# Performance work log

Measured on AMD Instinct MI355X. Metric: run time of the kernel, lower is better.

The kernel has to match this reference:

```python
import jax, jax.numpy as jnp
import numpy as np

EMB = 768
HEADS = 8
HEAD_DIM = EMB // HEADS  # 96
B, N = 4, 2048


def setup_inputs() -> dict:
    key = jax.random.key(0)
    ks = jax.random.split(key, 9)
    s = 1.0 / np.sqrt(EMB)
    x = jax.random.normal(ks[0], (B, N, EMB), dtype=jnp.float32)
    Wq = jax.random.uniform(ks[1], (EMB, EMB), jnp.float32, -s, s)
    bq = jax.random.uniform(ks[2], (EMB,), jnp.float32, -s, s)
    Wk = jax.random.uniform(ks[3], (EMB, EMB), jnp.float32, -s, s)
    bk = jax.random.uniform(ks[4], (EMB,), jnp.float32, -s, s)
    Wv = jax.random.uniform(ks[5], (EMB, EMB), jnp.float32, -s, s)
    bv = jax.random.uniform(ks[6], (EMB,), jnp.float32, -s, s)
    Wo = jax.random.uniform(ks[7], (EMB, EMB), jnp.float32, -s, s)
    bo = jax.random.uniform(ks[8], (EMB,), jnp.float32, -s, s)
    return {"x": x, "Wq": Wq, "bq": bq, "Wk": Wk, "bk": bk,
            "Wv": Wv, "bv": bv, "Wo": Wo, "bo": bo}


def _split_heads(t):
    b, n, _ = t.shape
    return t.reshape(b, n, HEADS, HEAD_DIM).transpose(0, 2, 1, 3)  # b h n d


def reference(x, Wq, bq, Wk, bk, Wv, bv, Wo, bo):
    q = _split_heads(x @ Wq + bq)
    k = _split_heads(x @ Wk + bk)
    v = _split_heads(x @ Wv + bv)
    # NOTE: faithful to source — softmax on UNSCALED logits, then divide by sqrt(head_dim)
    energy = jnp.einsum('bhqd,bhkd->bhqk', q, k)
    att = jax.nn.softmax(energy, axis=-1) / np.sqrt(HEAD_DIM)
    out = jnp.einsum('bhqk,bhkd->bhqd', att, v)
    out = out.transpose(0, 2, 1, 3).reshape(x.shape[0], x.shape[1], EMB)
    return out @ Wo + bo
```

## Files before the change

### kernel.cpp

```cpp
#include <hip/hip_runtime.h>

typedef _Float16 half_t;
typedef __attribute__((ext_vector_type(8))) _Float16 half8;
typedef __attribute__((ext_vector_type(2))) __fp16 fp16x2;
typedef __attribute__((ext_vector_type(4))) float f32x4;
typedef __attribute__((ext_vector_type(16))) float f32x16;

#define EMB 768
#define HEADS 8
#define HD 96
#define BB 4
#define NN 2048
#define BN (BB*NN)

static __device__ __forceinline__ f32x4 mfma16(half8 a, half8 b, f32x4 c) {
    return __builtin_amdgcn_mfma_f32_16x16x32_f16(a, b, c, 0, 0, 0);
}
static __device__ __forceinline__ f32x16 mfma32(half8 a, half8 b, f32x16 c) {
    return __builtin_amdgcn_mfma_f32_32x32x16_f16(a, b, c, 0, 0, 0);
}
static __device__ __forceinline__ unsigned pkrtz(float a, float b) {
    fp16x2 h = __builtin_amdgcn_cvt_pkrtz(a, b);
    return __builtin_bit_cast(unsigned, h);
}
static __device__ __forceinline__ unsigned sx32(unsigned v) {
    return (unsigned)__shfl_xor((int)v, 32);
}
static __device__ __forceinline__ float max3f(float a, float b, float c) {
    return fmaxf(fmaxf(a, b), c);
}
static __device__ __forceinline__ half8 pack8(float4 a, float4 b) {
    union { unsigned u[4]; half8 h; } t;
    t.u[0] = pkrtz(a.x, a.y); t.u[1] = pkrtz(a.z, a.w);
    t.u[2] = pkrtz(b.x, b.y); t.u[3] = pkrtz(b.z, b.w);
    return t.h;
}

__global__ __launch_bounds__(256) void cvt_transpose_w(
    const float* __restrict__ W0, const float* __restrict__ W1,
    const float* __restrict__ W2, const float* __restrict__ W3,
    half_t* __restrict__ T0, half_t* __restrict__ T1,
    half_t* __restrict__ T2, half_t* __restrict__ T3)
{
    const float* W; half_t* T;
    switch (blockIdx.z) {
        case 0: W = W0; T = T0; break;
        case 1: W = W1; T = T1; break;
        case 2: W = W2; T = T2; break;
        default: W = W3; T = T3; break;
    }
    __shared__ float ls[32][33];
    const int k0 = blockIdx.x * 32, n0 = blockIdx.y * 32;
    const int r = threadIdx.x >> 3, c4 = (threadIdx.x & 7) * 4;
    float4 v = *(const float4*)&W[(size_t)(k0 + r) * EMB + n0 + c4];
    ls[r][c4+0] = v.x; ls[r][c4+1] = v.y; ls[r][c4+2] = v.z; ls[r][c4+3] = v.w;
    __syncthreads();
    union { half_t h[4]; uint2 u; } t;
    #pragma unroll
    for (int j = 0; j < 4; ++j) t.h[j] = (half_t)ls[c4 + j][r];
    *(uint2*)&T[(size_t)(n0 + r) * EMB + k0 + c4] = t.u;
}

__global__ __launch_bounds__(256) void proj_qkv_h(
    const float* __restrict__ x,
    const half_t* __restrict__ WqT, const float* __restrict__ bq,
    const half_t* __restrict__ WkT, const float* __restrict__ bk,
    const half_t* __restrict__ WvT, const float* __restrict__ bv,
    half_t* __restrict__ Qo, half_t* __restrict__ Ko, half_t* __restrict__ Vt)
{
    const half_t* WT; const float* bias;
    const int z = blockIdx.z;
    if (z == 0)      { WT = WqT; bias = bq; }
    else if (z == 1) { WT = WkT; bias = bk; }
    else             { WT = WvT; bias = bv; }

    __shared__ half_t As[128][56];
    __shared__ half_t Bs[128][56];

    const int tid = threadIdx.x;
    const int lane = tid & 63;
    const int wid = tid >> 6;
    const int lr = lane & 15;
    const int lkg = lane >> 4;
    const int wm = (wid >> 1) * 64;
    const int wn = (wid & 1) * 64;
    const int mbase = blockIdx.x * 128;
    const int nbase = blockIdx.y * 128;

    const int srr = tid >> 2;
    const int skk = (tid & 3) * 8;

    f32x4 acc[4][4];
    const f32x4 z4 = {0.f, 0.f, 0.f, 0.f};
    #pragma unroll
    for (int i = 0; i < 4; ++i)
        #pragma unroll
        for (int j = 0; j < 4; ++j) acc[i][j] = z4;

    const float*  aptr = x  + (size_t)(mbase + srr) * EMB + skk;
    const half_t* bptr = WT + (size_t)(nbase + srr) * EMB + skk;

    half8 a0 = pack8(*(const float4*)(aptr),
                     *(const float4*)(aptr + 4));
    half8 a1 = pack8(*(const float4*)(aptr + 64 * EMB),
                     *(const float4*)(aptr + 64 * EMB + 4));
    half8 b0 = *(const half8*)bptr;
    half8 b1 = *(const half8*)(bptr + 64 * EMB);

    for (int k0 = 0; k0 < EMB; k0 += 32) {
        __syncthreads();
        *(half8*)&As[srr][skk]      = a0;
        *(half8*)&As[srr + 64][skk] = a1;
        *(half8*)&Bs[srr][skk]      = b0;
        *(half8*)&Bs[srr + 64][skk] = b1;
        __syncthreads();
        if (k0 + 32 < EMB) {
            a0 = pack8(*(const float4*)(aptr + k0 + 32),
                       *(const float4*)(aptr + k0 + 36));
            a1 = pack8(*(const float4*)(aptr + k0 + 32 + 64 * EMB),
                       *(const float4*)(aptr + k0 + 36 + 64 * EMB));
            b0 = *(const half8*)(bptr + k0 + 32);
            b1 = *(const half8*)(bptr + k0 + 32 + 64 * EMB);
        }
        half8 af[4], bf[4];
        #pragma unroll
        for (int mi = 0; mi < 4; ++mi)
            af[mi] = *(const half8*)&As[wm + mi*16 + lr][lkg*8];
        #pragma unroll
        for (int ni = 0; ni < 4; ++ni)
            bf[ni] = *(const half8*)&Bs[wn + ni*16 + lr][lkg*8];
        #pragma unroll
        for (int mi = 0; mi < 4; ++mi)
            #pragma unroll
            for (int ni = 0; ni < 4; ++ni)
                acc[mi][ni] = mfma16(af[mi], bf[ni], acc[mi][ni]);
    }

    const float qscale = (z == 0) ? 1.4426950408889634f : 1.0f;

    #pragma unroll
    for (int ni = 0; ni < 4; ++ni) {
        const int e = nbase + wn + ni*16 + lr;
        const float be = bias[e];
        const int h = e / HD, d = e % HD;
        #pragma unroll
        for (int mi = 0; mi < 4; ++mi) {
            const int row0 = mbase + wm + mi*16 + lkg*4;
            const int b = row0 >> 11, n0 = row0 & (NN - 1);
            if (z == 2) {
                union { half_t hh[4]; uint2 u; } t;
                #pragma unroll
                for (int r = 0; r < 4; ++r) t.hh[r] = (half_t)(acc[mi][ni][r] + be);
                *(uint2*)&Vt[((size_t)(b*HEADS + h) * HD + d) * NN + n0] = t.u;
            } else {
                half_t* outp = (z == 0) ? Qo : Ko;
                #pragma unroll
                for (int r = 0; r < 4; ++r)
                    outp[((size_t)(b*HEADS + h) * NN + n0 + r) * HD + d] =
                        (half_t)((acc[mi][ni][r] + be) * qscale);
            }
        }
    }
}

__global__ __launch_bounds__(256, 3) void attn_h(
    const half_t* __restrict__ Qh, const half_t* __restrict__ Kh,
    const half_t* __restrict__ Vth, half_t* __restrict__ AOh)
{
    __shared__ __align__(16) char smem[40960];

    const int tid = threadIdx.x;
    const int lane = tid & 63;
    const int wid = tid >> 6;
    const int l31 = lane & 31;
    const int b5 = lane >> 5;
    const int qsub = wid & 1;
    const int sub = wid >> 1;

    const int f = blockIdx.x;
    const int bh = (f & 7) + 8 * (f >> 8);
    const int qbase = ((f >> 3) & 31) * 64;

    const half_t* Qp = Qh + (size_t)bh * NN * HD;
    const half_t* Kp = Kh + (size_t)bh * NN * HD;
    const half_t* Vp = Vth + (size_t)bh * HD * NN;
    half_t* AOp = AOh + (size_t)bh * NN * HD;

    const int kr = tid >> 2;
    const int kcb = (tid & 3) * 48;
    const int vd = tid >> 1;
    const int vcb = (tid & 1) * 64;

    half8 kva, kvb, kvc, vv0, vv1, vv2, vv3;

#define KGLOAD(KT) {                                                          \
        const half_t* ksrc_ = Kp + (size_t)((KT) * 64 + kr) * HD + kcb / 2;   \
        kva = *(const half8*)(ksrc_);                                         \
        kvb = *(const half8*)(ksrc_ + 8);                                     \
        kvc = *(const half8*)(ksrc_ + 16); }
#define VGLOAD(KT) if (tid < 192) {                                           \
        const half_t* vsrc_ = Vp + (size_t)vd * NN + (KT) * 64 + vcb / 2;     \
        vv0 = *(const half8*)(vsrc_);      vv1 = *(const half8*)(vsrc_ + 8);  \
        vv2 = *(const half8*)(vsrc_ + 16); vv3 = *(const half8*)(vsrc_ + 24); }
#define WRITEBUF() {                                                          \
        char* kb_ = smem;                                                     \
        *(half8*)(kb_ + ((kr * 256 + kcb +  0) ^ ((kr & 15) << 4))) = kva;    \
        *(half8*)(kb_ + ((kr * 256 + kcb + 16) ^ ((kr & 15) << 4))) = kvb;    \
        *(half8*)(kb_ + ((kr * 256 + kcb + 32) ^ ((kr & 15) << 4))) = kvc;    \
        if (tid < 192) {                                                      \
            char* vb_ = smem + 16384;                                         \
            *(half8*)(vb_ + ((vd * 256 + vcb +  0) ^ ((vd & 15) << 4))) = vv0;\
            *(half8*)(vb_ + ((vd * 256 + vcb + 16) ^ ((vd & 15) << 4))) = vv1;\
            *(half8*)(vb_ + ((vd * 256 + vcb + 32) ^ ((vd & 15) << 4))) = vv2;\
            *(half8*)(vb_ + ((vd * 256 + vcb + 48) ^ ((vd & 15) << 4))) = vv3;\
        } }

    KGLOAD(0);
    VGLOAD(0);

    {
        const int r = tid >> 2;
        const int cb = (tid & 3) * 48;
        const half_t* src = Qp + (size_t)(qbase + r) * HD + cb / 2;
        #pragma unroll
        for (int c = 0; c < 3; ++c) {
            half8 q = *(const half8*)(src + c * 8);
            *(half8*)(smem + ((r * 256 + cb + c * 16) ^ ((r & 15) << 4))) = q;
        }
    }
    __syncthreads();
    half8 qf[6];
    {
        const int r = qsub * 32 + l31;
        #pragma unroll
        for (int kg = 0; kg < 6; ++kg)
            qf[kg] = *(const half8*)(smem + ((r * 256 + kg * 32 + 16 * b5) ^ ((r & 15) << 4)));
    }
    __syncthreads();

    f32x16 acc[3];
    const f32x16 z16 = {0.f,0.f,0.f,0.f,0.f,0.f,0.f,0.f,0.f,0.f,0.f,0.f,0.f,0.f,0.f,0.f};
    acc[0] = z16; acc[1] = z16; acc[2] = z16;
    float mreg = -1e30f, lreg = 0.f;

    const int kvrow = sub * 32 + l31;

    for (int kt = 0; kt < NN / 64; ++kt) {
        WRITEBUF();
        __syncthreads();

        if (kt + 1 < NN / 64) {
            KGLOAD(kt + 1);
            VGLOAD(kt + 1);
        }

        f32x16 st = z16;
        __builtin_amdgcn_s_setprio(1);
        #pragma unroll
        for (int kg = 0; kg < 6; ++kg) {
            half8 kf = *(const half8*)(smem +
                ((kvrow * 256 + kg * 32 + 16 * b5) ^ ((kvrow & 15) << 4)));
            st = mfma32(kf, qf[kg], st);
        }
        __builtin_amdgcn_s_setprio(0);

        const float t0 = max3f(st[0],  st[1],  st[2]);
        const float t1 = max3f(st[3],  st[4],  st[5]);
        const float t2 = max3f(st[6],  st[7],  st[8]);
        const float t3 = max3f(st[9],  st[10], st[11]);
        const float t4 = max3f(st[12], st[13], st[14]);
        const float tml = fmaxf(max3f(t0, t1, t2), max3f(t3, t4, st[15]));
        const float tm = fmaxf(tml, __shfl_xor(tml, 32));

        if (!__all(tm <= mreg + 8.0f)) {
            const float mn = fmaxf(mreg, tm);
            const float sc = exp2f(mreg - mn);
            lreg *= sc;
            #pragma unroll
            for (int db = 0; db < 3; ++db)
                #pragma unroll
                for (int i = 0; i < 16; ++i) acc[db][i] *= sc;
            mreg = mn;
        }

        float rs = 0.f;
        #pragma unroll
        for (int i = 0; i < 16; ++i) {
            const float p = exp2f(st[i] - mreg);
            st[i] = p;
            rs += p;
        }
        rs += __shfl_xor(rs, 32);
        lreg += rs;

        unsigned pk[4][2];
        #pragma unroll
        for (int rr = 0; rr < 4; ++rr) {
            pk[rr][0] = pkrtz(st[rr*4+0], st[rr*4+1]);
            pk[rr][1] = pkrtz(st[rr*4+2], st[rr*4+3]);
        }

        #pragma unroll
        for (int ks = 0; ks < 2; ++ks) {
            const unsigned z0 = b5 ? pk[2*ks][0] : pk[2*ks+1][0];
            const unsigned z1 = b5 ? pk[2*ks][1] : pk[2*ks+1][1];
            const unsigned x0 = sx32(z0);
            const unsigned x1 = sx32(z1);
            union { unsigned u[4]; half8 h; } afu;
            afu.u[0] = b5 ? x0 : pk[2*ks][0];
            afu.u[1] = b5 ? x1 : pk[2*ks][1];
            afu.u[2] = b5 ? pk[2*ks+1][0] : x0;
            afu.u[3] = b5 ? pk[2*ks+1][1] : x1;
            const half8 af = afu.h;
            __builtin_amdgcn_s_setprio(1);
            #pragma unroll
            for (int db = 0; db < 3; ++db) {
                const int d = db * 32 + l31;
                half8 vf = *(const half8*)(smem + 16384 +
                    ((d * 256 + sub * 64 + ks * 32 + 16 * b5) ^ ((d & 15) << 4)));
                acc[db] = mfma32(vf, af, acc[db]);
            }
            __builtin_amdgcn_s_setprio(0);
        }
        __syncthreads();
    }

#undef KGLOAD
#undef VGLOAD
#undef WRITEBUF

    float* fb = (float*)smem;
    fb[tid] = mreg;
    fb[256 + tid] = lreg;
    __syncthreads();
    const float mp = fb[tid ^ 128];
    const float lp = fb[256 + (tid ^ 128)];
    const float mc = fmaxf(mreg, mp);
    const float sc = exp2f(mreg - mc);
    const float lc = lreg * sc + lp * exp2f(mp - mc);
    __syncthreads();
    if (wid >= 2) {
        float* rec = fb + (qsub * 64 + lane) * 49;
        #pragma unroll
        for (int db = 0; db < 3; ++db)
            #pragma unroll
            for (int i = 0; i < 16; ++i) rec[db*16 + i] = acc[db][i] * sc;
    }
    __syncthreads();
    if (wid < 2) {
        const float* rec = fb + (qsub * 64 + lane) * 49;
        const float isq = 0.10206207261596577f;
        const float inv = isq / lc;
        const int q = qbase + qsub * 32 + l31;
        half_t* dst = AOp + (size_t)q * HD;
        #pragma unroll
        for (int db = 0; db < 3; ++db)
            #pragma unroll
            for (int rr = 0; rr < 4; ++rr) {
                const int d0 = db * 32 + rr * 8 + 4 * b5;
                union { half_t h[4]; uint2 u; } t;
                #pragma unroll
                for (int r = 0; r < 4; ++r)
                    t.h[r] = (half_t)((acc[db][rr*4 + r] * sc + rec[db*16 + rr*4 + r]) * inv);
                *(uint2*)&dst[d0] = t.u;
            }
    }
}

__global__ __launch_bounds__(256) void proj_out_h(
    const half_t* __restrict__ AOh, const half_t* __restrict__ WoT,
    const float* __restrict__ bo, float* __restrict__ out)
{
    __shared__ half_t As[128][56];
    __shared__ half_t Bs[128][56];

    const int tid = threadIdx.x;
    const int lane = tid & 63;
    const int wid = tid >> 6;
    const int lr = lane & 15;
    const int lkg = lane >> 4;
    const int wm = (wid >> 1) * 64;
    const int wn = (wid & 1) * 64;
    const int mbase = blockIdx.x * 128;
    const int nbase = blockIdx.y * 128;

    const int srr = tid >> 2;
    const int skk = (tid & 3) * 8;

    const int arow0 = mbase + srr;
    const int ab0 = arow0 >> 11, an0 = arow0 & (NN - 1);
    const int arow1 = arow0 + 64;
    const int ab1 = arow1 >> 11, an1 = arow1 & (NN - 1);

    f32x4 acc[4][4];
    const f32x4 z4 = {0.f, 0.f, 0.f, 0.f};
    #pragma unroll
    for (int i = 0; i < 4; ++i)
        #pragma unroll
        for (int j = 0; j < 4; ++j) acc[i][j] = z4;

    const half_t* bptr = WoT + (size_t)(nbase + srr) * EMB + skk;

#define ALOAD(b_, n_, k0_) \
    (*(const half8*)&AOh[((size_t)((b_)*HEADS + (k0_)/HD) * NN + (n_)) * HD + ((k0_)%HD) + skk])

    half8 a0 = ALOAD(ab0, an0, 0);
    half8 a1 = ALOAD(ab1, an1, 0);
    half8 b0 = *(const half8*)bptr;
    half8 b1 = *(const half8*)(bptr + 64 * EMB);

    for (int k0 = 0; k0 < EMB; k0 += 32) {
        __syncthreads();
        *(half8*)&As[srr][skk]      = a0;
        *(half8*)&As[srr + 64][skk] = a1;
        *(half8*)&Bs[srr][skk]      = b0;
        *(half8*)&Bs[srr + 64][skk] = b1;
        __syncthreads();
        if (k0 + 32 < EMB) {
            const int kn = k0 + 32;
            a0 = ALOAD(ab0, an0, kn);
            a1 = ALOAD(ab1, an1, kn);
            b0 = *(const half8*)(bptr + kn);
            b1 = *(const half8*)(bptr + kn + 64 * EMB);
        }
        half8 af[4], bf[4];
        #pragma unroll
        for (int mi = 0; mi < 4; ++mi)
            af[mi] = *(const half8*)&As[wm + mi*16 + lr][lkg*8];
        #pragma unroll
        for (int ni = 0; ni < 4; ++ni)
            bf[ni] = *(const half8*)&Bs[wn + ni*16 + lr][lkg*8];
        #pragma unroll
        for (int mi = 0; mi < 4; ++mi)
            #pragma unroll
            for (int ni = 0; ni < 4; ++ni)
                acc[mi][ni] = mfma16(af[mi], bf[ni], acc[mi][ni]);
    }
#undef ALOAD

    #pragma unroll
    for (int ni = 0; ni < 4; ++ni) {
        const int e = nbase + wn + ni*16 + lr;
        const float be = bo[e];
        #pragma unroll
        for (int mi = 0; mi < 4; ++mi) {
            const int row0 = mbase + wm + mi*16 + lkg*4;
            #pragma unroll
            for (int r = 0; r < 4; ++r)
                out[(size_t)(row0 + r) * EMB + e] = acc[mi][ni][r] + be;
        }
    }
}

extern "C" void kernel_launch(void* const* d_in, const int* in_sizes, int n_in,
                              void* d_out, int out_size, void* d_ws, size_t ws_size,
                              hipStream_t stream)
{
    const float* x  = (const float*)d_in[0];
    const float* Wq = (const float*)d_in[1];
    const float* bq = (const float*)d_in[2];
    const float* Wk = (const float*)d_in[3];
    const float* bk = (const float*)d_in[4];
    const float* Wv = (const float*)d_in[5];
    const float* bv = (const float*)d_in[6];
    const float* Wo = (const float*)d_in[7];
    const float* bo = (const float*)d_in[8];

    const size_t SZ = (size_t)BN * EMB;
    const size_t WS = (size_t)EMB * EMB;

    half_t* ws  = (half_t*)d_ws;
    half_t* WqT = ws;
    half_t* WkT = WqT + WS;
    half_t* WvT = WkT + WS;
    half_t* WoT = WvT + WS;
    half_t* Qh  = WoT + WS;
    half_t* Kh  = Qh  + SZ;
    half_t* Vth = Kh  + SZ;
    half_t* AOh = Vth + SZ;

    cvt_transpose_w<<<dim3(EMB/32, EMB/32, 4), 256, 0, stream>>>(
        Wq, Wk, Wv, Wo, WqT, WkT, WvT, WoT);

    proj_qkv_h<<<dim3(BN/128, EMB/128, 3), 256, 0, stream>>>(
        x, WqT, bq, WkT, bk, WvT, bv, Qh, Kh, Vth);

    attn_h<<<dim3((NN/64) * (BB*HEADS)), 256, 0, stream>>>(Qh, Kh, Vth, AOh);

    proj_out_h<<<dim3(BN/128, EMB/128), 256, 0, stream>>>(AOh, WoT, bo, (float*)d_out);
}
```

Baseline: 167.8 us.

## Process 128 queries per attention block, sharing K/V fragments across two subtiles

Each attention block now covers 128 queries instead of 64, and each wave computes two 32-query subtiles against the same K and V fragments read from shared memory. The goal is to halve the global and LDS traffic for K/V per query and to put more MFMA work behind each load. In exchange, register pressure roughly doubles for accumulators and Q fragments. The launch bound drops to 2 blocks per CU, and the grid is halved to 512 blocks, which reduces latency hiding and tail balance. The epilogue merges the two wave halves once per subtile, adding extra barriers.

```diff
diff --git a/kernel.cpp b/kernel.cpp
--- a/kernel.cpp
+++ b/kernel.cpp
@@ -163,7 +163,7 @@
     }
 }
 
-__global__ __launch_bounds__(256, 3) void attn_h(
+__global__ __launch_bounds__(256, 2) void attn_h(
     const half_t* __restrict__ Qh, const half_t* __restrict__ Kh,
     const half_t* __restrict__ Vth, half_t* __restrict__ AOh)
 {
@@ -178,8 +178,8 @@
     const int sub = wid >> 1;
 
     const int f = blockIdx.x;
-    const int bh = (f & 7) + 8 * (f >> 8);
-    const int qbase = ((f >> 3) & 31) * 64;
+    const int bh = (f & 7) + 8 * (f >> 7);
+    const int qbase = ((f >> 3) & 15) * 128;
 
     const half_t* Qp = Qh + (size_t)bh * NN * HD;
     const half_t* Kp = Kh + (size_t)bh * NN * HD;
@@ -219,29 +219,35 @@
     VGLOAD(0);
 
     {
-        const int r = tid >> 2;
-        const int cb = (tid & 3) * 48;
+        const int r = tid >> 1;
+        const int cb = (tid & 1) * 96;
         const half_t* src = Qp + (size_t)(qbase + r) * HD + cb / 2;
         #pragma unroll
-        for (int c = 0; c < 3; ++c) {
-            half8 q = *(const half8*)(src + c * 8);
+        for (int c = 0; c < 6; ++c) {
+            half8 q = *(const half8*)(src + c * 16 / 2);
             *(half8*)(smem + ((r * 256 + cb + c * 16) ^ ((r & 15) << 4))) = q;
         }
     }
     __syncthreads();
-    half8 qf[6];
-    {
-        const int r = qsub * 32 + l31;
+    half8 qf[2][6];
+    #pragma unroll
+    for (int s = 0; s < 2; ++s) {
+        const int r = qsub * 64 + s * 32 + l31;
         #pragma unroll
         for (int kg = 0; kg < 6; ++kg)
-            qf[kg] = *(const half8*)(smem + ((r * 256 + kg * 32 + 16 * b5) ^ ((r & 15) << 4)));
+            qf[s][kg] = *(const half8*)(smem +
+                ((r * 256 + kg * 32 + 16 * b5) ^ ((r & 15) << 4)));
     }
     __syncthreads();
 
-    f32x16 acc[3];
+    f32x16 acc[2][3];
     const f32x16 z16 = {0.f,0.f,0.f,0.f,0.f,0.f,0.f,0.f,0.f,0.f,0.f,0.f,0.f,0.f,0.f,0.f};
-    acc[0] = z16; acc[1] = z16; acc[2] = z16;
-    float mreg = -1e30f, lreg = 0.f;
+    #pragma unroll
+    for (int s = 0; s < 2; ++s) {
+        acc[s][0] = z16; acc[s][1] = z16; acc[s][2] = z16;
+    }
+    float mreg[2] = {-1e30f, -1e30f};
+    float lreg[2] = {0.f, 0.f};
 
     const int kvrow = sub * 32 + l31;
 
@@ -254,71 +260,81 @@
             VGLOAD(kt + 1);
         }
 
-        f32x16 st = z16;
+        f32x16 st[2];
+        st[0] = z16; st[1] = z16;
         __builtin_amdgcn_s_setprio(1);
         #pragma unroll
         for (int kg = 0; kg < 6; ++kg) {
             half8 kf = *(const half8*)(smem +
                 ((kvrow * 256 + kg * 32 + 16 * b5) ^ ((kvrow & 15) << 4)));
-            st = mfma32(kf, qf[kg], st);
+            st[0] = mfma32(kf, qf[0][kg], st[0]);
+            st[1] = mfma32(kf, qf[1][kg], st[1]);
         }
         __builtin_amdgcn_s_setprio(0);
 
-        const float t0 = max3f(st[0],  st[1],  st[2]);
-        const float t1 = max3f(st[3],  st[4],  st[5]);
-        const float t2 = max3f(st[6],  st[7],  st[8]);
-        const float t3 = max3f(st[9],  st[10], st[11]);
-        const float t4 = max3f(st[12], st[13], st[14]);
-        const float tml = fmaxf(max3f(t0, t1, t2), max3f(t3, t4, st[15]));
-        const float tm = fmaxf(tml, __shfl_xor(tml, 32));
-
-        if (!__all(tm <= mreg + 8.0f)) {
-            const float mn = fmaxf(mreg, tm);
-            const float sc = exp2f(mreg - mn);
-            lreg *= sc;
-            #pragma unroll
-            for (int db = 0; db < 3; ++db)
+        unsigned pk[2][4][2];
+        #pragma unroll
+        for (int s = 0; s < 2; ++s) {
+            const float t0 = max3f(st[s][0],  st[s][1],  st[s][2]);
+            const float t1 = max3f(st[s][3],  st[s][4],  st[s][5]);
+            const float t2 = max3f(st[s][6],  st[s][7],  st[s][8]);
+            const float t3 = max3f(st[s][9],  st[s][10], st[s][11]);
+            const float t4 = max3f(st[s][12], st[s][13], st[s][14]);
+            const float tml = fmaxf(max3f(t0, t1, t2), max3f(t3, t4, st[s][15]));
+            const float tm = fmaxf(tml, __shfl_xor(tml, 32));
+
+            if (!__all(tm <= mreg[s] + 8.0f)) {
+                const float mn = fmaxf(mreg[s], tm);
+                const float sc = exp2f(mreg[s] - mn);
+                lreg[s] *= sc;
                 #pragma unroll
-                for (int i = 0; i < 16; ++i) acc[db][i] *= sc;
-            mreg = mn;
-        }
-
-        float rs = 0.f;
-        #pragma unroll
-        for (int i = 0; i < 16; ++i) {
-            const float p = exp2f(st[i] - mreg);
-            st[i] = p;
-            rs += p;
-        }
-        rs += __shfl_xor(rs, 32);
-        lreg += rs;
-
-        unsigned pk[4][2];
-        #pragma unroll
-        for (int rr = 0; rr < 4; ++rr) {
-            pk[rr][0] = pkrtz(st[rr*4+0], st[rr*4+1]);
-            pk[rr][1] = pkrtz(st[rr*4+2], st[rr*4+3]);
+                for (int db = 0; db < 3; ++db)
+                    #pragma unroll
+                    for (int i = 0; i < 16; ++i) acc[s][db][i] *= sc;
+                mreg[s] = mn;
+            }
+
+            float rs = 0.f;
+            #pragma unroll
+            for (int i = 0; i < 16; ++i) {
+                const float p = exp2f(st[s][i] - mreg[s]);
+                st[s][i] = p;
+                rs += p;
+            }
+            rs += __shfl_xor(rs, 32);
+            lreg[s] += rs;
+
+            #pragma unroll
+            for (int rr = 0; rr < 4; ++rr) {
+                pk[s][rr][0] = pkrtz(st[s][rr*4+0], st[s][rr*4+1]);
+                pk[s][rr][1] = pkrtz(st[s][rr*4+2], st[s][rr*4+3]);
+            }
         }
 
         #pragma unroll
         for (int ks = 0; ks < 2; ++ks) {
-            const unsigned z0 = b5 ? pk[2*ks][0] : pk[2*ks+1][0];
-            const unsigned z1 = b5 ? pk[2*ks][1] : pk[2*ks+1][1];
-            const unsigned x0 = sx32(z0);
-            const unsigned x1 = sx32(z1);
-            union { unsigned u[4]; half8 h; } afu;
-            afu.u[0] = b5 ? x0 : pk[2*ks][0];
-            afu.u[1] = b5 ? x1 : pk[2*ks][1];
-            afu.u[2] = b5 ? pk[2*ks+1][0] : x0;
-            afu.u[3] = b5 ? pk[2*ks+1][1] : x1;
-            const half8 af = afu.h;
+            half8 af[2];
+            #pragma unroll
+            for (int s = 0; s < 2; ++s) {
+                const unsigned z0 = b5 ? pk[s][2*ks][0] : pk[s][2*ks+1][0];
+                const unsigned z1 = b5 ? pk[s][2*ks][1] : pk[s][2*ks+1][1];
+                const unsigned x0 = sx32(z0);
+                const unsigned x1 = sx32(z1);
+                union { unsigned u[4]; half8 h; } afu;
+                afu.u[0] = b5 ? x0 : pk[s][2*ks][0];
+                afu.u[1] = b5 ? x1 : pk[s][2*ks][1];
+                afu.u[2] = b5 ? pk[s][2*ks+1][0] : x0;
+                afu.u[3] = b5 ? pk[s][2*ks+1][1] : x1;
+                af[s] = afu.h;
+            }
             __builtin_amdgcn_s_setprio(1);
             #pragma unroll
             for (int db = 0; db < 3; ++db) {
                 const int d = db * 32 + l31;
                 half8 vf = *(const half8*)(smem + 16384 +
                     ((d * 256 + sub * 64 + ks * 32 + 16 * b5) ^ ((d & 15) << 4)));
-                acc[db] = mfma32(vf, af, acc[db]);
+                acc[0][db] = mfma32(vf, af[0], acc[0][db]);
+                acc[1][db] = mfma32(vf, af[1], acc[1][db]);
             }
             __builtin_amdgcn_s_setprio(0);
         }
@@ -329,41 +345,45 @@
 #undef VGLOAD
 #undef WRITEBUF
 
+    const float isq = 0.10206207261596577f;
     float* fb = (float*)smem;
-    fb[tid] = mreg;
-    fb[256 + tid] = lreg;
-    __syncthreads();
-    const float mp = fb[tid ^ 128];
-    const float lp = fb[256 + (tid ^ 128)];
-    const float mc = fmaxf(mreg, mp);
-    const float sc = exp2f(mreg - mc);
-    const float lc = lreg * sc + lp * exp2f(mp - mc);
-    __syncthreads();
-    if (wid >= 2) {
-        float* rec = fb + (qsub * 64 + lane) * 49;
-        #pragma unroll
-        for (int db = 0; db < 3; ++db)
-            #pragma unroll
-            for (int i = 0; i < 16; ++i) rec[db*16 + i] = acc[db][i] * sc;
-    }
-    __syncthreads();
-    if (wid < 2) {
-        const float* rec = fb + (qsub * 64 + lane) * 49;
-        const float isq = 0.10206207261596577f;
-        const float inv = isq / lc;
-        const int q = qbase + qsub * 32 + l31;
-        half_t* dst = AOp + (size_t)q * HD;
-        #pragma unroll
-        for (int db = 0; db < 3; ++db)
-            #pragma unroll
-            for (int rr = 0; rr < 4; ++rr) {
-                const int d0 = db * 32 + rr * 8 + 4 * b5;
-                union { half_t h[4]; uint2 u; } t;
+    #pragma unroll
+    for (int s = 0; s < 2; ++s) {
+        __syncthreads();
+        fb[tid] = mreg[s];
+        fb[256 + tid] = lreg[s];
+        __syncthreads();
+        const float mp = fb[tid ^ 128];
+        const float lp = fb[256 + (tid ^ 128)];
+        const float mc = fmaxf(mreg[s], mp);
+        const float sc = exp2f(mreg[s] - mc);
+        const float lc = lreg[s] * sc + lp * exp2f(mp - mc);
+        __syncthreads();
+        if (wid >= 2) {
+            float* rec = fb + (qsub * 64 + lane) * 49;
+            #pragma unroll
+            for (int db = 0; db < 3; ++db)
                 #pragma unroll
-                for (int r = 0; r < 4; ++r)
-                    t.h[r] = (half_t)((acc[db][rr*4 + r] * sc + rec[db*16 + rr*4 + r]) * inv);
-                *(uint2*)&dst[d0] = t.u;
-            }
+                for (int i = 0; i < 16; ++i) rec[db*16 + i] = acc[s][db][i] * sc;
+        }
+        __syncthreads();
+        if (wid < 2) {
+            const float* rec = fb + (qsub * 64 + lane) * 49;
+            const float inv = isq / lc;
+            const int q = qbase + qsub * 64 + s * 32 + l31;
+            half_t* dst = AOp + (size_t)q * HD;
+            #pragma unroll
+            for (int db = 0; db < 3; ++db)
+                #pragma unroll
+                for (int rr = 0; rr < 4; ++rr) {
+                    const int d0 = db * 32 + rr * 8 + 4 * b5;
+                    union { half_t h[4]; uint2 u; } t;
+                    #pragma unroll
+                    for (int r = 0; r < 4; ++r)
+                        t.h[r] = (half_t)((acc[s][db][rr*4 + r] * sc + rec[db*16 + rr*4 + r]) * inv);
+                    *(uint2*)&dst[d0] = t.u;
+                }
+        }
     }
 }
 
@@ -485,7 +505,7 @@
     proj_qkv_h<<<dim3(BN/128, EMB/128, 3), 256, 0, stream>>>(
         x, WqT, bq, WkT, bk, WvT, bv, Qh, Kh, Vth);
 
-    attn_h<<<dim3((NN/64) * (BB*HEADS)), 256, 0, stream>>>(Qh, Kh, Vth, AOh);
+    attn_h<<<dim3((NN/128) * (BB*HEADS)), 256, 0, stream>>>(Qh, Kh, Vth, AOh);
 
     proj_out_h<<<dim3(BN/128, EMB/128), 256, 0, stream>>>(AOh, WoT, bo, (float*)d_out);
 }
```

Result: faster. 156.6 us (-6.6%).
